# Kernel optimization log

Measured on AMD Instinct MI355X. Metric: run time of the kernel, lower is better.

The kernel has to match this reference:

```python
import jax, jax.numpy as jnp
import numpy as np

B, S, NQ = 32, 200, 10000
ED, H = 256, 512
NF = 19  # repeated(7) + seq(6) + past(6)


def setup_inputs() -> dict:
    key = jax.random.key(0)
    ks = jax.random.split(key, 24)
    f32 = jnp.float32
    def n(k, shape, scale=0.05):
        return jax.random.normal(k, shape, dtype=f32) * scale
    inp = {}
    inp['x_data'] = jax.random.randint(ks[0], (B, S), 0, 2 * NQ + 1)
    inp['q_t_data'] = jax.random.randint(ks[1], (B * S,), 0, NQ + 1)
    inp['target'] = jax.random.uniform(ks[2], (B * S,), dtype=f32)
    inp['repeated_time_gap'] = jax.random.uniform(ks[3], (B, S + 1, 7), dtype=f32)
    inp['past_trail_counts'] = jax.random.uniform(ks[4], (B, S + 1, 6), dtype=f32)
    inp['seq_time_gap'] = jax.random.uniform(ks[5], (B, S + 1, 6), dtype=f32)
    # learned parameters
    inp['embed'] = n(ks[6], (2 * NQ + 1, ED)).at[0].set(0.0)  # padding_idx=0
    inp['W_ih0'] = n(ks[7], (4 * H, ED + NF))
    inp['W_hh0'] = n(ks[8], (4 * H, H))
    inp['b_ih0'] = n(ks[9], (4 * H,))
    inp['b_hh0'] = n(ks[10], (4 * H,))
    inp['W_ih1'] = n(ks[11], (4 * H, H))
    inp['W_hh1'] = n(ks[12], (4 * H, H))
    inp['b_ih1'] = n(ks[13], (4 * H,))
    inp['b_hh1'] = n(ks[14], (4 * H,))
    inp['W_pred'] = n(ks[15], (NQ + 1, H + NF))
    inp['b_pred'] = jnp.zeros((NQ + 1,), dtype=f32)
    inp['C'] = n(ks[16], (B, S, NF), scale=1.0)
    inp['init_h'] = n(ks[17], (2, B, H), scale=1.0)
    inp['init_c'] = n(ks[18], (2, B, H), scale=1.0)
    return inp


def _lstm_layer(x, h0, c0, Wih, Whh, bih, bhh):
    # x: [B, S, D] batch_first; scan over time (PyTorch gate order i,f,g,o)
    def step(carry, xt):
        h, cc = carry
        g = xt @ Wih.T + h @ Whh.T + bih + bhh  # [B, 4H]
        i, f, gg, o = jnp.split(g, 4, axis=-1)
        cc = jax.nn.sigmoid(f) * cc + jax.nn.sigmoid(i) * jnp.tanh(gg)
        h = jax.nn.sigmoid(o) * jnp.tanh(cc)
        return (h, cc), h
    _, hs = jax.lax.scan(step, (h0, c0), jnp.swapaxes(x, 0, 1))
    return jnp.swapaxes(hs, 0, 1)  # [B, S, H]


def reference(x_data, q_t_data, target, repeated_time_gap, past_trail_counts,
              seq_time_gap, embed, W_ih0, W_hh0, b_ih0, b_hh0, W_ih1, W_hh1,
              b_ih1, b_hh1, W_pred, b_pred, C, init_h, init_c):
    # c: [B, S+1, 19]
    c = jnp.concatenate([repeated_time_gap, seq_time_gap, past_trail_counts], axis=2)
    c_t = C * c[:, :-1, :]
    x_emb = embed[x_data]  # [B, S, ED]
    inp = jnp.concatenate([x_emb, c_t], axis=2)  # [B, S, ED+19]
    h1 = _lstm_layer(inp, init_h[0], init_c[0], W_ih0, W_hh0, b_ih0, b_hh0)
    lstm_out = _lstm_layer(h1, init_h[1], init_c[1], W_ih1, W_hh1, b_ih1, b_hh1)
    c_next = C * c[:, 1:, :]
    pi = jnp.concatenate([lstm_out, c_next], axis=2).reshape(B * S, H + NF)
    # dropout is identity in eval mode
    pred = pi @ W_pred.T + b_pred  # [B*S, NQ+1]
    # fused per-row gather (replaces the Python loop over chunks)
    pred_1d = jnp.take_along_axis(pred, q_t_data[:, None], axis=1)[:, 0]
    mask = (q_t_data > 0).astype(pred_1d.dtype)
    x, t = pred_1d, target
    # stable BCE-with-logits, mean over masked entries
    bce = jnp.maximum(x, 0.0) - x * t + jnp.log1p(jnp.exp(-jnp.abs(x)))
    loss = jnp.sum(bce * mask) / jnp.sum(mask)
    return loss, jax.nn.sigmoid(pred_1d) * mask, t * mask
```

## Files before the change

### kernel.cpp

```cpp
#include <hip/hip_runtime.h>
#include <hip/hip_bf16.h>

#define B_   32
#define S_   200
#define H_   512
#define ED_  256
#define NF_  19
#define NROW (B_*S_)
#define G4H  (4*H_)
#define KIN  (ED_+NF_)
#define KP_  288
#define ALD  296

typedef __attribute__((ext_vector_type(8))) short short8;
typedef __attribute__((ext_vector_type(4))) float f32x4;
typedef __attribute__((ext_vector_type(4))) unsigned int u32x4;

#define OFF_G0   0ull
#define SZ_G0    ((size_t)NROW*G4H*4)
#define OFF_LSTM (OFF_G0 + SZ_G0)
#define SZ_LSTM  ((size_t)NROW*H_*4)
#define OFF_CT   (OFF_LSTM + SZ_LSTM)
#define SZ_CT    ((size_t)NROW*NF_*4)
#define OFF_CN   (OFF_CT + SZ_CT)
#define OFF_H0   (OFF_CN + SZ_CT)
#define SZ_HB    ((size_t)2*B_*H_*2)
#define OFF_H1   (OFF_H0 + SZ_HB)
#define OFF_SYNC (OFF_H1 + SZ_HB)
#define OFF_WB   (OFF_SYNC + 8192)
#define SZ_WB    ((size_t)G4H*KP_*2)

__device__ __forceinline__ unsigned short f2bf(float f) {
    unsigned u = __float_as_uint(f);
    unsigned r = u + 0x7fffu + ((u >> 16) & 1u);
    return (unsigned short)(r >> 16);
}
__device__ __forceinline__ float sigf(float x) { return 1.0f / (1.0f + __expf(-x)); }

#define CLD16(d, p, o) \
    asm volatile("global_load_dwordx4 %0, %1, off offset:" o " sc0 sc1" \
                 : "=v"(d) : "v"(p))
#define CLDPLANE(F, b) do { \
    const unsigned short* _pa = (b) + 2048; \
    const unsigned short* _pb = (b) + 6144; \
    CLD16(F[0],_pa,"-4096"); CLD16(F[1],_pa,"-3072"); CLD16(F[2],_pa,"-2048"); CLD16(F[3],_pa,"-1024"); \
    CLD16(F[4],_pa,"0");     CLD16(F[5],_pa,"1024");  CLD16(F[6],_pa,"2048");  CLD16(F[7],_pa,"3072");  \
    CLD16(F[8],_pb,"-4096"); CLD16(F[9],_pb,"-3072"); CLD16(F[10],_pb,"-2048");CLD16(F[11],_pb,"-1024");\
    CLD16(F[12],_pb,"0");    CLD16(F[13],_pb,"1024"); CLD16(F[14],_pb,"2048"); CLD16(F[15],_pb,"3072"); \
} while (0)
#define CST128(a, v) \
    asm volatile("global_store_dwordx4 %0, %1, off sc0 sc1" :: "v"(a), "v"(v) : "memory")
#define PLD32(d, p, o) \
    asm volatile("global_load_dword %0, %1, off offset:" o : "=v"(d) : "v"(p))


__global__ __launch_bounds__(256) void prep_kernel(
    const float* __restrict__ C, const float* __restrict__ rep,
    const float* __restrict__ past, const float* __restrict__ seq,
    const float* __restrict__ init_h,
    float* __restrict__ ct, float* __restrict__ cn,
    unsigned short* __restrict__ h0buf, unsigned short* __restrict__ h1buf,
    unsigned* __restrict__ syncbuf)
{
    int idx = blockIdx.x * 256 + threadIdx.x;
    if (idx < NROW * NF_) {
        int m = idx % NF_; int row = idx / NF_;
        int b = row / S_, s = row % S_;
        float cc = C[idx];
        float v0, v1;
        if (m < 7)       { v0 = rep [(b*(S_+1)+s)*7 + m];      v1 = rep [(b*(S_+1)+s+1)*7 + m]; }
        else if (m < 13) { v0 = seq [(b*(S_+1)+s)*6 + (m-7)];  v1 = seq [(b*(S_+1)+s+1)*6 + (m-7)]; }
        else             { v0 = past[(b*(S_+1)+s)*6 + (m-13)]; v1 = past[(b*(S_+1)+s+1)*6 + (m-13)]; }
        ct[idx] = cc * v0;
        cn[idx] = cc * v1;
    }
    int j = idx - NROW * NF_;
    if (j >= 0 && j < B_ * H_) {
        int b = j >> 9, u = j & (H_ - 1);
        int fi = ((b >> 4) * 8192) + ((u >> 5) * 512)
               + ((((u >> 3) & 3) * 16 + (b & 15)) * 8) + (u & 7);
        h0buf[fi] = f2bf(init_h[j]);
        h1buf[fi] = f2bf(init_h[B_ * H_ + j]);
    }
    if (j >= B_ * H_ && j < B_ * H_ + 1100) syncbuf[j - B_ * H_] = 0u;
}

__global__ __launch_bounds__(256) void prepw_kernel(
    const float* __restrict__ Wih0, unsigned short* __restrict__ wb)
{
    int idx = blockIdx.x * 256 + threadIdx.x;
    if (idx >= G4H * KP_) return;
    int k = idx % KP_; int r = idx / KP_;
    wb[idx] = (k < KIN) ? f2bf(Wih0[(size_t)r * KIN + k]) : (unsigned short)0;
}

__global__ __launch_bounds__(256) void g0_kernel(
    const int* __restrict__ x_data, const float* __restrict__ embed,
    const unsigned short* __restrict__ wb,
    const float* __restrict__ bih0, const float* __restrict__ bhh0,
    const float* __restrict__ ct, float* __restrict__ G0)
{
    __shared__ unsigned short A[32 * ALD];
    int tid = threadIdx.x;
    int bx = blockIdx.x;
    int mb = bx >> 5;
    int nb = bx & 31;
    int rbase = mb * 32;
    {
        int r = tid >> 3, c8 = tid & 7;
        int grow = rbase + r;
        const float* erow = embed + (size_t)x_data[grow] * ED_;
        #pragma unroll
        for (int jj = 0; jj < 8; jj++) {
            float4 v = *(const float4*)(erow + c8 * 32 + jj * 4);
            unsigned short* d = &A[r * ALD + c8 * 32 + jj * 4];
            d[0] = f2bf(v.x); d[1] = f2bf(v.y); d[2] = f2bf(v.z); d[3] = f2bf(v.w);
        }
        if (c8 == 0) {
            const float* crow = ct + (size_t)grow * NF_;
            for (int m = 0; m < NF_; m++) A[r * ALD + ED_ + m] = f2bf(crow[m]);
            for (int m = NF_; m < 32; m++) A[r * ALD + ED_ + m] = 0;
        }
    }
    __syncthreads();
    int lane = tid & 63, w = tid >> 6;
    int ncol = nb * 64 + w * 16 + (lane & 15);
    int kb = (lane >> 4) * 8;
    f32x4 acc0 = {0.f,0.f,0.f,0.f}, acc1 = {0.f,0.f,0.f,0.f};
    #pragma unroll
    for (int ks = 0; ks < 9; ks++) {
        int k0 = ks * 32 + kb;
        short8 bfr = *(const short8*)(wb + (size_t)ncol * KP_ + k0);
        short8 a0 = *(const short8*)&A[(lane & 15) * ALD + k0];
        short8 a1 = *(const short8*)&A[(16 + (lane & 15)) * ALD + k0];
        acc0 = __builtin_amdgcn_mfma_f32_16x16x32_bf16(a0, bfr, acc0, 0, 0, 0);
        acc1 = __builtin_amdgcn_mfma_f32_16x16x32_bf16(a1, bfr, acc1, 0, 0, 0);
    }
    float bias = bih0[ncol] + bhh0[ncol];
    #pragma unroll
    for (int r = 0; r < 4; r++) {
        int row0 = (lane >> 4) * 4 + r;
        G0[(size_t)(rbase + row0) * G4H + ncol]      = acc0[r] + bias;
        G0[(size_t)(rbase + 16 + row0) * G4H + ncol] = acc1[r] + bias;
    }
}

__global__ __launch_bounds__(256, 1) void scan_kernel(
    const float* __restrict__ G0,
    const float* __restrict__ Whh0,
    const float* __restrict__ Wih1, const float* __restrict__ Whh1,
    const float* __restrict__ bih1, const float* __restrict__ bhh1,
    const float* __restrict__ init_c,
    unsigned short* __restrict__ h0buf, unsigned short* __restrict__ h1buf,
    float* __restrict__ lstm_out,
    unsigned* __restrict__ bar)
{
    __shared__ float g0l[32 * 33];
    __shared__ float g1l[32 * 33];
    __shared__ float c0s[8 * 33];
    __shared__ float c1s[8 * 33];
    __shared__ float bias1[32];

    int tid = threadIdx.x;
    int p = blockIdx.x;
    int lane = tid & 63, w = tid >> 6;
    int mt = w & 1, nt = w >> 1;
    int lr = nt * 16 + (lane & 15);
    int gr = (lr >> 3) * H_ + p * 8 + (lr & 7);
    int kb = (lane >> 4) * 8;

    unsigned* flagw = bar + 64;

    short8 B0[16], B1[32];
    #pragma unroll
    for (int ks = 0; ks < 16; ks++) {
        const float* s0 = Whh0 + (size_t)gr * H_ + ks * 32 + kb;
        const float* s1 = Wih1 + (size_t)gr * H_ + ks * 32 + kb;
        const float* s2 = Whh1 + (size_t)gr * H_ + ks * 32 + kb;
        float4 a = *(const float4*)(s0), b = *(const float4*)(s0 + 4);
        short8 t0; t0[0]=f2bf(a.x);t0[1]=f2bf(a.y);t0[2]=f2bf(a.z);t0[3]=f2bf(a.w);
                   t0[4]=f2bf(b.x);t0[5]=f2bf(b.y);t0[6]=f2bf(b.z);t0[7]=f2bf(b.w);
        B0[ks] = t0;
        a = *(const float4*)(s1); b = *(const float4*)(s1 + 4);
        short8 t1; t1[0]=f2bf(a.x);t1[1]=f2bf(a.y);t1[2]=f2bf(a.z);t1[3]=f2bf(a.w);
                   t1[4]=f2bf(b.x);t1[5]=f2bf(b.y);t1[6]=f2bf(b.z);t1[7]=f2bf(b.w);
        B1[ks] = t1;
        a = *(const float4*)(s2); b = *(const float4*)(s2 + 4);
        short8 t2; t2[0]=f2bf(a.x);t2[1]=f2bf(a.y);t2[2]=f2bf(a.z);t2[3]=f2bf(a.w);
                   t2[4]=f2bf(b.x);t2[5]=f2bf(b.y);t2[6]=f2bf(b.z);t2[7]=f2bf(b.w);
        B1[16 + ks] = t2;
    }
    if (tid < 32) {
        int g = (tid >> 3) * H_ + p * 8 + (tid & 7);
        bias1[tid] = bih1[g] + bhh1[g];
    }
    int uu = tid & 7, b8 = tid >> 3;
    c0s[uu * 33 + b8] = init_c[(size_t)b8 * H_ + p * 8 + uu];
    c1s[uu * 33 + b8] = init_c[(size_t)B_ * H_ + (size_t)b8 * H_ + p * 8 + uu];
    __syncthreads();

    const float* gptr = G0 + (size_t)b8 * S_ * G4H + p * 8 + uu + 2 * H_;
    int sidx = ((b8 >> 4) * 8192) + ((p >> 2) * 512) + (((p & 3) * 16 + (b8 & 15)) * 8);

    for (int it = 0; it <= S_; it++) {
        float gpre0 = 0.f, gpre1 = 0.f, gpre2 = 0.f, gpre3 = 0.f;
        if (it < S_) {
            const float* gsrc = gptr + (size_t)it * G4H;
            PLD32(gpre0, gsrc, "-4096");
            PLD32(gpre1, gsrc, "-2048");
            PLD32(gpre2, gsrc, "0");
            PLD32(gpre3, gsrc, "2048");
        }
        if (it) {
            unsigned tgt = (unsigned)it;
            const unsigned* fp = flagw + lane * 16;
            for (;;) {
                unsigned fvv;
                asm volatile("global_load_dword %0, %1, off sc0 sc1" : "=v"(fvv) : "v"(fp));
                asm volatile("s_waitcnt vmcnt(0)" : "+v"(fvv));
                if (__all((int)(fvv >= tgt))) break;
                __builtin_amdgcn_s_sleep(1);
            }
        }
        const unsigned short* b0p = h0buf + (it & 1) * 16384 + mt * 8192 + lane * 8;
        const unsigned short* b1p = h1buf + ((it + 1) & 1) * 16384 + mt * 8192 + lane * 8;
        short8 F0[16], F1[16];
        CLDPLANE(F0, b0p);
        CLDPLANE(F1, b1p);

        asm volatile("s_waitcnt vmcnt(0)"
            : "+v"(F0[0]),"+v"(F0[1]),"+v"(F0[2]),"+v"(F0[3]),
              "+v"(F0[4]),"+v"(F0[5]),"+v"(F0[6]),"+v"(F0[7]),
              "+v"(F0[8]),"+v"(F0[9]),"+v"(F0[10]),"+v"(F0[11]),
              "+v"(F0[12]),"+v"(F0[13]),"+v"(F0[14]),"+v"(F0[15]),
              "+v"(F1[0]),"+v"(F1[1]),"+v"(F1[2]),"+v"(F1[3]),
              "+v"(F1[4]),"+v"(F1[5]),"+v"(F1[6]),"+v"(F1[7]),
              "+v"(F1[8]),"+v"(F1[9]),"+v"(F1[10]),"+v"(F1[11]),
              "+v"(F1[12]),"+v"(F1[13]),"+v"(F1[14]),"+v"(F1[15]),
              "+v"(gpre0),"+v"(gpre1),"+v"(gpre2),"+v"(gpre3));

        f32x4 acc0 = {0.f,0.f,0.f,0.f};
        f32x4 a1a  = {0.f,0.f,0.f,0.f};
        f32x4 a1b  = {0.f,0.f,0.f,0.f};
        #pragma unroll
        for (int ks = 0; ks < 16; ks++) {
            acc0 = __builtin_amdgcn_mfma_f32_16x16x32_bf16(F0[ks], B0[ks],      acc0, 0, 0, 0);
            a1a  = __builtin_amdgcn_mfma_f32_16x16x32_bf16(F0[ks], B1[ks],      a1a,  0, 0, 0);
            a1b  = __builtin_amdgcn_mfma_f32_16x16x32_bf16(F1[ks], B1[16 + ks], a1b,  0, 0, 0);
        }
        #pragma unroll
        for (int r = 0; r < 4; r++) {
            int row = mt * 16 + (lane >> 4) * 4 + r;
            g0l[row * 33 + lr] = acc0[r];
            g1l[row * 33 + lr] = a1a[r] + a1b[r];
        }
        __syncthreads();

        if (it < S_) {
            float iv = g0l[b8 * 33 + uu]       + gpre0;
            float fv = g0l[b8 * 33 + 8 + uu]   + gpre1;
            float gv = g0l[b8 * 33 + 16 + uu]  + gpre2;
            float ov = g0l[b8 * 33 + 24 + uu]  + gpre3;
            float c = c0s[uu * 33 + b8];
            c = sigf(fv) * c + sigf(iv) * tanhf(gv);
            c0s[uu * 33 + b8] = c;
            float h = sigf(ov) * tanhf(c);
            unsigned short hb = f2bf(h);
            float hn = __shfl_down(h, 1, 64);
            unsigned pk = (unsigned)hb | ((unsigned)f2bf(hn) << 16);
            unsigned q  = (unsigned)__shfl_down((int)pk, 2, 64);
            unsigned r0 = (unsigned)__shfl_down((int)pk, 4, 64);
            unsigned r1 = (unsigned)__shfl_down((int)q,  4, 64);
            if (!(tid & 7)) {
                u32x4 val = {pk, q, r0, r1};
                unsigned short* dst = h0buf + ((it + 1) & 1) * 16384 + sidx;
                CST128(dst, val);
            }
        }
        float h1out = 0.f;
        if (it >= 1) {
            float iv = g1l[b8 * 33 + uu]       + bias1[uu];
            float fv = g1l[b8 * 33 + 8 + uu]   + bias1[8 + uu];
            float gv = g1l[b8 * 33 + 16 + uu]  + bias1[16 + uu];
            float ov = g1l[b8 * 33 + 24 + uu]  + bias1[24 + uu];
            float c = c1s[uu * 33 + b8];
            c = sigf(fv) * c + sigf(iv) * tanhf(gv);
            c1s[uu * 33 + b8] = c;
            float h = sigf(ov) * tanhf(c);
            h1out = h;
            unsigned short hb = f2bf(h);
            float hn = __shfl_down(h, 1, 64);
            unsigned pk = (unsigned)hb | ((unsigned)f2bf(hn) << 16);
            unsigned q  = (unsigned)__shfl_down((int)pk, 2, 64);
            unsigned r0 = (unsigned)__shfl_down((int)pk, 4, 64);
            unsigned r1 = (unsigned)__shfl_down((int)q,  4, 64);
            if (!(tid & 7)) {
                u32x4 val = {pk, q, r0, r1};
                unsigned short* dst = h1buf + (it & 1) * 16384 + sidx;
                CST128(dst, val);
            }
        }

        if (it < S_) {
            asm volatile("s_waitcnt vmcnt(0)" ::: "memory");
            __syncthreads();
            if (tid == 0) {
                unsigned fv = (unsigned)(it + 1);
                unsigned* fp = flagw + p * 16;
                asm volatile("global_store_dword %0, %1, off sc0 sc1"
                             :: "v"(fp), "v"(fv) : "memory");
            }
        }
        if (it >= 1) {
            lstm_out[(size_t)(b8 * S_ + (it - 1)) * H_ + p * 8 + uu] = h1out;
        }
    }
}

__global__ __launch_bounds__(256) void pred_kernel(
    const float* __restrict__ lstm_out, const float* __restrict__ cn,
    const float* __restrict__ Wp, const float* __restrict__ bp,
    const int* __restrict__ qt, const float* __restrict__ target,
    float* __restrict__ out, float* __restrict__ accum)
{
    int wv = (blockIdx.x * 256 + threadIdx.x) >> 6;
    int lane = threadIdx.x & 63;
    if (wv >= NROW) return;
    int q = qt[wv];
    const float* wrow = Wp + (size_t)q * (H_ + NF_);
    const float* hrow = lstm_out + (size_t)wv * H_;
    float part = 0.f;
    #pragma unroll
    for (int i = 0; i < H_ / 64; i++) part += hrow[lane + i * 64] * wrow[lane + i * 64];
    if (lane < NF_) part += cn[(size_t)wv * NF_ + lane] * wrow[H_ + lane];
    #pragma unroll
    for (int off = 32; off; off >>= 1) part += __shfl_down(part, off, 64);
    if (lane == 0) {
        float x = part + bp[q];
        float t = target[wv];
        float mask = (q > 0) ? 1.f : 0.f;
        out[1 + wv] = mask / (1.f + __expf(-x));
        out[1 + NROW + wv] = t * mask;
        float bce = fmaxf(x, 0.f) - x * t + log1pf(__expf(-fabsf(x)));
        atomicAdd(&accum[0], bce * mask);
        atomicAdd(&accum[1], mask);
    }
}

__global__ void final_kernel(const float* __restrict__ accum, float* __restrict__ out)
{
    out[0] = accum[0] / accum[1];
}

extern "C" void kernel_launch(void* const* d_in, const int* in_sizes, int n_in,
                              void* d_out, int out_size, void* d_ws, size_t ws_size,
                              hipStream_t stream)
{
    (void)in_sizes; (void)n_in; (void)out_size; (void)ws_size;
    const int*   x_data = (const int*)  d_in[0];
    const int*   q_t    = (const int*)  d_in[1];
    const float* target = (const float*)d_in[2];
    const float* rep    = (const float*)d_in[3];
    const float* past   = (const float*)d_in[4];
    const float* seq    = (const float*)d_in[5];
    const float* embed  = (const float*)d_in[6];
    const float* Wih0   = (const float*)d_in[7];
    const float* Whh0   = (const float*)d_in[8];
    const float* bih0   = (const float*)d_in[9];
    const float* bhh0   = (const float*)d_in[10];
    const float* Wih1   = (const float*)d_in[11];
    const float* Whh1   = (const float*)d_in[12];
    const float* bih1   = (const float*)d_in[13];
    const float* bhh1   = (const float*)d_in[14];
    const float* Wp     = (const float*)d_in[15];
    const float* bp     = (const float*)d_in[16];
    const float* C      = (const float*)d_in[17];
    const float* init_h = (const float*)d_in[18];
    const float* init_c = (const float*)d_in[19];

    char* ws = (char*)d_ws;
    float*          G0    = (float*)         (ws + OFF_G0);
    float*          lstm  = (float*)         (ws + OFF_LSTM);
    float*          ct    = (float*)         (ws + OFF_CT);
    float*          cn    = (float*)         (ws + OFF_CN);
    unsigned short* h0buf = (unsigned short*)(ws + OFF_H0);
    unsigned short* h1buf = (unsigned short*)(ws + OFF_H1);
    unsigned*       sync  = (unsigned*)      (ws + OFF_SYNC);
    unsigned short* wb    = (unsigned short*)(ws + OFF_WB);
    float* out = (float*)d_out;

    prep_kernel<<<544, 256, 0, stream>>>(C, rep, past, seq, init_h, ct, cn, h0buf, h1buf, sync);
    prepw_kernel<<<(G4H * KP_ + 255) / 256, 256, 0, stream>>>(Wih0, wb);
    g0_kernel<<<6400, 256, 0, stream>>>(x_data, embed, wb, bih0, bhh0, ct, G0);
    scan_kernel<<<64, 256, 0, stream>>>(G0, Whh0, Wih1, Whh1, bih1, bhh1, init_c,
                                        h0buf, h1buf, lstm, sync);
    pred_kernel<<<NROW / 4, 256, 0, stream>>>(lstm, cn, Wp, bp, q_t, target, out,
                                              (float*)sync);
    final_kernel<<<1, 1, 0, stream>>>((const float*)sync, out);
}
```

Baseline: 1.151 ms.

## Stage recurrent hidden states through LDS and poll flags with a single wave

In the persistent scan kernel, only wave 0 now spins on the cross-block flags and releases the other waves through an LDS variable. The hidden-state vectors are loaded once cooperatively by all 256 threads into LDS, replacing the old scheme where each wave loaded its full half-plane redundantly. MFMA operands are then read from LDS. This cuts duplicated global/L2 traffic and polling pressure on the critical per-step path, at the cost of an extra __syncthreads, an LDS round trip and 64KB of shared memory.

```diff
diff --git a/kernel.cpp b/kernel.cpp
--- a/kernel.cpp
+++ b/kernel.cpp
@@ -40,14 +40,6 @@
 #define CLD16(d, p, o) \
     asm volatile("global_load_dwordx4 %0, %1, off offset:" o " sc0 sc1" \
                  : "=v"(d) : "v"(p))
-#define CLDPLANE(F, b) do { \
-    const unsigned short* _pa = (b) + 2048; \
-    const unsigned short* _pb = (b) + 6144; \
-    CLD16(F[0],_pa,"-4096"); CLD16(F[1],_pa,"-3072"); CLD16(F[2],_pa,"-2048"); CLD16(F[3],_pa,"-1024"); \
-    CLD16(F[4],_pa,"0");     CLD16(F[5],_pa,"1024");  CLD16(F[6],_pa,"2048");  CLD16(F[7],_pa,"3072");  \
-    CLD16(F[8],_pb,"-4096"); CLD16(F[9],_pb,"-3072"); CLD16(F[10],_pb,"-2048");CLD16(F[11],_pb,"-1024");\
-    CLD16(F[12],_pb,"0");    CLD16(F[13],_pb,"1024"); CLD16(F[14],_pb,"2048"); CLD16(F[15],_pb,"3072"); \
-} while (0)
 #define CST128(a, v) \
     asm volatile("global_store_dwordx4 %0, %1, off sc0 sc1" :: "v"(a), "v"(v) : "memory")
 #define PLD32(d, p, o) \
@@ -155,11 +147,14 @@
     float* __restrict__ lstm_out,
     unsigned* __restrict__ bar)
 {
+    __shared__ unsigned short h0l[16384];
+    __shared__ unsigned short h1l[16384];
     __shared__ float g0l[32 * 33];
     __shared__ float g1l[32 * 33];
     __shared__ float c0s[8 * 33];
     __shared__ float c1s[8 * 33];
     __shared__ float bias1[32];
+    __shared__ unsigned rel;
 
     int tid = threadIdx.x;
     int p = blockIdx.x;
@@ -194,6 +189,7 @@
         int g = (tid >> 3) * H_ + p * 8 + (tid & 7);
         bias1[tid] = bih1[g] + bhh1[g];
     }
+    if (tid == 0) rel = 0u;
     int uu = tid & 7, b8 = tid >> 3;
     c0s[uu * 33 + b8] = init_c[(size_t)b8 * H_ + p * 8 + uu];
     c1s[uu * 33 + b8] = init_c[(size_t)B_ * H_ + (size_t)b8 * H_ + p * 8 + uu];
@@ -213,40 +209,57 @@
         }
         if (it) {
             unsigned tgt = (unsigned)it;
-            const unsigned* fp = flagw + lane * 16;
-            for (;;) {
-                unsigned fvv;
-                asm volatile("global_load_dword %0, %1, off sc0 sc1" : "=v"(fvv) : "v"(fp));
-                asm volatile("s_waitcnt vmcnt(0)" : "+v"(fvv));
-                if (__all((int)(fvv >= tgt))) break;
-                __builtin_amdgcn_s_sleep(1);
-            }
-        }
-        const unsigned short* b0p = h0buf + (it & 1) * 16384 + mt * 8192 + lane * 8;
-        const unsigned short* b1p = h1buf + ((it + 1) & 1) * 16384 + mt * 8192 + lane * 8;
-        short8 F0[16], F1[16];
-        CLDPLANE(F0, b0p);
-        CLDPLANE(F1, b1p);
-
-        asm volatile("s_waitcnt vmcnt(0)"
-            : "+v"(F0[0]),"+v"(F0[1]),"+v"(F0[2]),"+v"(F0[3]),
-              "+v"(F0[4]),"+v"(F0[5]),"+v"(F0[6]),"+v"(F0[7]),
-              "+v"(F0[8]),"+v"(F0[9]),"+v"(F0[10]),"+v"(F0[11]),
-              "+v"(F0[12]),"+v"(F0[13]),"+v"(F0[14]),"+v"(F0[15]),
-              "+v"(F1[0]),"+v"(F1[1]),"+v"(F1[2]),"+v"(F1[3]),
-              "+v"(F1[4]),"+v"(F1[5]),"+v"(F1[6]),"+v"(F1[7]),
-              "+v"(F1[8]),"+v"(F1[9]),"+v"(F1[10]),"+v"(F1[11]),
-              "+v"(F1[12]),"+v"(F1[13]),"+v"(F1[14]),"+v"(F1[15]),
-              "+v"(gpre0),"+v"(gpre1),"+v"(gpre2),"+v"(gpre3));
+            if (w == 0) {
+                const unsigned* fp = flagw + lane * 16;
+                for (;;) {
+                    unsigned fvv;
+                    asm volatile("global_load_dword %0, %1, off sc0 sc1" : "=v"(fvv) : "v"(fp));
+                    asm volatile("s_waitcnt vmcnt(0)" : "+v"(fvv));
+                    if (__all((int)(fvv >= tgt))) break;
+                    __builtin_amdgcn_s_sleep(1);
+                }
+                if (lane == 0)
+                    __hip_atomic_store(&rel, tgt, __ATOMIC_RELAXED, __HIP_MEMORY_SCOPE_WORKGROUP);
+            } else {
+                while (__hip_atomic_load(&rel, __ATOMIC_RELAXED, __HIP_MEMORY_SCOPE_WORKGROUP) < tgt)
+                    __builtin_amdgcn_s_sleep(1);
+            }
+        }
+        {
+            const unsigned short* g0p = h0buf + (it & 1) * 16384 + tid * 8;
+            const unsigned short* g1p = h1buf + ((it + 1) & 1) * 16384 + tid * 8;
+            short8 sv0[8], sv1[8];
+            #pragma unroll
+            for (int k = 0; k < 4; k++) {
+                CLD16(sv0[2*k],   g0p + (2*k+1)*2048, "-4096");
+                CLD16(sv0[2*k+1], g0p + (2*k+1)*2048, "0");
+                CLD16(sv1[2*k],   g1p + (2*k+1)*2048, "-4096");
+                CLD16(sv1[2*k+1], g1p + (2*k+1)*2048, "0");
+            }
+            asm volatile("s_waitcnt vmcnt(0)"
+                : "+v"(sv0[0]),"+v"(sv0[1]),"+v"(sv0[2]),"+v"(sv0[3]),
+                  "+v"(sv0[4]),"+v"(sv0[5]),"+v"(sv0[6]),"+v"(sv0[7]),
+                  "+v"(sv1[0]),"+v"(sv1[1]),"+v"(sv1[2]),"+v"(sv1[3]),
+                  "+v"(sv1[4]),"+v"(sv1[5]),"+v"(sv1[6]),"+v"(sv1[7]),
+                  "+v"(gpre0),"+v"(gpre1),"+v"(gpre2),"+v"(gpre3));
+            #pragma unroll
+            for (int k = 0; k < 8; k++) {
+                *(short8*)&h0l[tid * 8 + k * 2048] = sv0[k];
+                *(short8*)&h1l[tid * 8 + k * 2048] = sv1[k];
+            }
+        }
+        __syncthreads();
 
         f32x4 acc0 = {0.f,0.f,0.f,0.f};
         f32x4 a1a  = {0.f,0.f,0.f,0.f};
         f32x4 a1b  = {0.f,0.f,0.f,0.f};
         #pragma unroll
         for (int ks = 0; ks < 16; ks++) {
-            acc0 = __builtin_amdgcn_mfma_f32_16x16x32_bf16(F0[ks], B0[ks],      acc0, 0, 0, 0);
-            a1a  = __builtin_amdgcn_mfma_f32_16x16x32_bf16(F0[ks], B1[ks],      a1a,  0, 0, 0);
-            a1b  = __builtin_amdgcn_mfma_f32_16x16x32_bf16(F1[ks], B1[16 + ks], a1b,  0, 0, 0);
+            short8 f0 = *(const short8*)&h0l[mt * 8192 + ks * 512 + lane * 8];
+            short8 f1 = *(const short8*)&h1l[mt * 8192 + ks * 512 + lane * 8];
+            acc0 = __builtin_amdgcn_mfma_f32_16x16x32_bf16(f0, B0[ks],      acc0, 0, 0, 0);
+            a1a  = __builtin_amdgcn_mfma_f32_16x16x32_bf16(f0, B1[ks],      a1a,  0, 0, 0);
+            a1b  = __builtin_amdgcn_mfma_f32_16x16x32_bf16(f1, B1[16 + ks], a1b,  0, 0, 0);
         }
         #pragma unroll
         for (int r = 0; r < 4; r++) {
```

New measurement: 1.184 ms. +2.9%, slower.
